# Optimization experiments

Measured on AMD Instinct MI355X. Metric: run time of the kernel, lower is better.

The kernel has to match this reference:

```python
import jax, jax.numpy as jnp
import numpy as np

N_IMG = 512
N_ANGLES = 180


def _bilinear(img, sy, sx):
    """Bilinear sample img at float coords (sy, sx); zero outside the image."""
    n = img.shape[0]
    y0 = jnp.floor(sy)
    x0 = jnp.floor(sx)
    wy = sy - y0
    wx = sx - x0
    y0i = y0.astype(jnp.int32)
    x0i = x0.astype(jnp.int32)

    def gather(yi, xi):
        valid = (yi >= 0) & (yi < n) & (xi >= 0) & (xi < n)
        yc = jnp.clip(yi, 0, n - 1)
        xc = jnp.clip(xi, 0, n - 1)
        return jnp.where(valid, img[yc, xc], jnp.zeros((), img.dtype))

    v00 = gather(y0i, x0i)
    v01 = gather(y0i, x0i + 1)
    v10 = gather(y0i + 1, x0i)
    v11 = gather(y0i + 1, x0i + 1)
    return (v00 * (1 - wy) * (1 - wx) + v01 * (1 - wy) * wx
            + v10 * wy * (1 - wx) + v11 * wy * wx)


def _radon(img, angles):
    """skimage-style radon: rotate image by each angle, sum along axis 0.
    Returns sinogram of shape (n_detectors, n_angles) = (N, len(angles))."""
    n = img.shape[0]
    c = (n - 1) * 0.5  # rotation about image center
    coords = jnp.arange(n, dtype=img.dtype) - c
    yc, xc = jnp.meshgrid(coords, coords, indexing="ij")  # (N, N)

    def one_angle(theta_deg):
        t = jnp.deg2rad(theta_deg.astype(img.dtype))
        co, si = jnp.cos(t), jnp.sin(t)
        # inverse-rotation sampling coordinates (CCW rotation of the image)
        sx = co * xc + si * yc + c
        sy = -si * xc + co * yc + c
        rotated = _bilinear(img, sy, sx)  # (N, N)
        return rotated.sum(axis=0)        # projection along detector rows -> (N,)

    sino = jax.vmap(one_angle)(angles)  # (n_angles, N)
    return sino.T                        # (N, n_angles)


def setup_inputs() -> dict:
    key = jax.random.key(0)
    img = jax.random.uniform(key, (N_IMG, N_IMG), dtype=jnp.float32)  # nonnegative PET activity
    angles = jnp.arange(N_ANGLES, dtype=jnp.int32)  # degrees 0..179 (skimage default)
    return {"img": img, "angles": angles}


def reference(img, angles):
    return _radon(img, angles)
```

## Files before the change

kernel.cpp:

```cpp
#include <hip/hip_runtime.h>
#include <hip/hip_fp16.h>
#include <stdint.h>

#define N 512
#define NA 180
#define TD 64
#define TI 128
#define TW 96
#define TILE_DW (36 * 256)
#define PP 708
#define PR 704
#define POFF 96

#define WS_IMGPB  0
#define WS_IMGTPB (PR * PP)
#define WS_TAB    (2 * PR * PP)
#define WS_FLAGS  (WS_TAB + 4 * NA)
#define WS_OUTT   997888

typedef _Float16 hh2 __attribute__((ext_vector_type(2)));
union H2U { uint32_t u; hh2 h; };

__device__ __forceinline__ hh2 cvt_pkrtz(float a, float b) {
    return __builtin_bit_cast(hh2, __builtin_amdgcn_cvt_pkrtz(a, b));
}

__device__ __forceinline__ void load16_to_lds(const uint32_t* g, uint32_t* l) {
    __builtin_amdgcn_global_load_lds(
        (const __attribute__((address_space(1))) void*)g,
        (__attribute__((address_space(3))) void*)l,
        16 , 0 , 0 );
}

__global__ __launch_bounds__(512) void pad_kernel(const float* __restrict__ img,
                                                  const int* __restrict__ angles,
                                                  uint32_t* __restrict__ imgPB,
                                                  uint32_t* __restrict__ imgTPB,
                                                  float4* __restrict__ tab,
                                                  int* __restrict__ flags,
                                                  float* __restrict__ outT) {
    __shared__ float lds[65 * 66];
    const int tid  = threadIdx.x;
    const int lane = tid & 63;
    const int wq   = tid >> 6;
    const int bx = blockIdx.x, by = blockIdx.y;
    const int b  = by * 11 + bx;

    if (b < 45) {
        float4 z; z.x = z.y = z.z = z.w = 0.0f;
        ((float4*)outT)[b * 512 + tid] = z;
    }
    if (b == 120 && tid < NA) {
        float t = (float)angles[tid] * 0.017453292519943295f;
        float si = sinf(t), co = cosf(t);
        int useT = fabsf(si) > fabsf(co);
        float4 e;
        if (useT) { e.x = co; e.y = -si; e.z = si; e.w = co; }
        else      { e.x = si; e.y = co;  e.z = co; e.w = -si; }
        tab[tid] = e;
        flags[tid] = useT;
    }

    for (int idx = tid; idx < 65 * 65; idx += 512) {
        int r = idx / 65, cc = idx - r * 65;
        int y = by * 64 + r - POFF, x = bx * 64 + cc - POFF;
        bool in = ((unsigned)y < N) && ((unsigned)x < N);
        lds[r * 66 + cc] = in ? img[y * N + x] : 0.0f;
    }
    __syncthreads();
#pragma unroll
    for (int j = 0; j < 8; ++j) {
        int r = wq * 8 + j;
        float v0 = lds[r * 66 + lane], v1 = lds[r * 66 + lane + 1];
        __half2 h = __halves2half2(__float2half(v0), __float2half(v1));
        imgPB[(size_t)(by * 64 + r) * PP + bx * 64 + lane] = *(uint32_t*)&h;
        float t0 = lds[lane * 66 + r], t1 = lds[(lane + 1) * 66 + r];
        __half2 ht = __halves2half2(__float2half(t0), __float2half(t1));
        imgTPB[(size_t)(bx * 64 + r) * PP + by * 64 + lane] = *(uint32_t*)&ht;
    }
}

__global__ __launch_bounds__(512, 8) void radon_kernel(const uint32_t* __restrict__ imgPB,
                                                       const uint32_t* __restrict__ imgTPB,
                                                       const float4* __restrict__ tab,
                                                       const int* __restrict__ flags,
                                                       float* __restrict__ outT) {
    __shared__ uint32_t tile[TILE_DW];

    const int tid  = threadIdx.x;
    const int lane = tid & 63;
    const int wave = tid >> 6;
    const int d0 = blockIdx.x * TD;
    const int a  = blockIdx.y;
    const int i0 = blockIdx.z * TI;

    const float c = 255.5f;
    const float4 tb = tab[a];
    const float au = tb.x, bus = tb.y, av = tb.z, bvs = tb.w;

    const float xc0 = (float)d0 - c, xc1 = (float)(d0 + TD - 1) - c;
    const float buA = fmaf(bus, xc0, c), buB = fmaf(bus, xc1, c);
    const float bvA = fmaf(bvs, xc0, c), bvB = fmaf(bvs, xc1, c);
    const float buMin = fminf(buA, buB), buMax = fmaxf(buA, buB);
    const float bvMin = fminf(bvA, bvB), bvMax = fmaxf(bvA, bvB);

    {
        const float fi0 = (float)i0 - c, fi1 = (float)(i0 + TI - 1) - c;
        const float fiLoU = (au >= 0.0f) ? fi0 : fi1, fiHiU = (au >= 0.0f) ? fi1 : fi0;
        const float fiLoV = (av >= 0.0f) ? fi0 : fi1, fiHiV = (av >= 0.0f) ? fi1 : fi0;
        if (fmaf(au, fiLoU, buMin) > (float)N || fmaf(au, fiHiU, buMax) < -1.0f ||
            fmaf(av, fiLoV, bvMin) > (float)N || fmaf(av, fiHiV, bvMax) < -1.0f)
            return;
    }

    const uint32_t* __restrict__ src = flags[a] ? imgTPB : imgPB;

    const float xcl = (float)(d0 + lane) - c;
    const float buLb = fmaf(bus, xcl, c);
    const float bvLb = fmaf(bvs, xcl, c);

    const int t0g  = wave * 256 + (lane << 2);
    const int q0   = t0g / TW;
    const int c0   = t0g - q0 * TW;
    const int goff0 = q0 * PP + c0;

    float s = 0.0f;
#pragma unroll
    for (int ph = 0; ph < 2; ++ph) {
        const int ip = i0 + ph * 64;
        const float fi0 = (float)ip - c, fi1 = (float)(ip + 63) - c;
        const float fiLoU = (au >= 0.0f) ? fi0 : fi1, fiHiU = (au >= 0.0f) ? fi1 : fi0;
        const float fiLoV = (av >= 0.0f) ? fi0 : fi1, fiHiV = (av >= 0.0f) ? fi1 : fi0;
        const float umin = fmaf(au, fiLoU, buMin), umax = fmaf(au, fiHiU, buMax);
        const float vmin = fmaf(av, fiLoV, bvMin), vmax = fmaf(av, fiHiV, bvMax);
        const bool live = !(umin > (float)N || umax < -1.0f ||
                            vmin > (float)N || vmax < -1.0f);

        const int ub0 = (((int)floorf(umin)) - 1) & ~3;
        const int vb  = ((int)floorf(vmin)) - 1;

        __syncthreads();
        if (live) {
            const uint32_t* gb = src + (vb + POFF) * PP + (ub0 + POFF) + goff0;
            int cc = c0;
#pragma unroll
            for (int st = 0; st < 5; ++st) {
                int chunk = st * 8 + wave;
                if (chunk < 36) load16_to_lds(gb, &tile[chunk * 256]);
                cc += 32;
                int wrap = (cc >= TW);
                cc = wrap ? cc - TW : cc;
                gb += 21 * PP + 32 + (wrap ? (PP - TW) : 0);
            }
        }
        __syncthreads();
        if (live) {
            const float buL = buLb - (float)ub0;
            const float bvL = bvLb - (float)vb;
            const float fiw = (float)(ip + wave * 8) - c;
            float u = fmaf(au, fiw, buL);
            float v = fmaf(av, fiw, bvL);
#pragma unroll
            for (int k = 0; k < 8; ++k) {
                float wx = __builtin_amdgcn_fractf(u);
                float wy = __builtin_amdgcn_fractf(v);
                int iu = (int)u, iv = (int)v;
                int ai = iv * TW + iu;
                H2U P0, P1;
                P0.u = tile[ai];
                P1.u = tile[ai + TW];
                hh2 wy2 = cvt_pkrtz(wy, wy);
                hh2 m   = wy2 * (P1.h - P0.h) + P0.h;
                hh2 wv  = cvt_pkrtz(1.0f - wx, wx);
                s = __builtin_amdgcn_fdot2(wv, m, s, false);
                u += au;
                v += av;
            }
        }
    }

    __syncthreads();
    float* ft = (float*)tile;
    ft[tid] = s;
    __syncthreads();
    if (tid < 64) {
        float r = ft[tid]       + ft[tid + 64]  + ft[tid + 128] + ft[tid + 192]
                + ft[tid + 256] + ft[tid + 320] + ft[tid + 384] + ft[tid + 448];
        atomicAdd(&outT[a * 512 + d0 + tid], r);
    }
}

__global__ __launch_bounds__(256) void txo_kernel(const float* __restrict__ outT,
                                                  float* __restrict__ out) {
    __shared__ float lds[64 * 65];
    const int lane = threadIdx.x & 63;
    const int wq   = threadIdx.x >> 6;
    const int d0 = blockIdx.x * 64;
    const int a0 = blockIdx.y * 64;
#pragma unroll
    for (int j = 0; j < 16; ++j) {
        int r = wq * 16 + j;
        int a = a0 + r;
        lds[r * 65 + lane] = (a < NA) ? outT[a * 512 + d0 + lane] : 0.0f;
    }
    __syncthreads();
#pragma unroll
    for (int j = 0; j < 16; ++j) {
        int r = wq * 16 + j;
        int aa = a0 + lane;
        if (aa < NA) out[(d0 + r) * NA + aa] = lds[lane * 65 + r];
    }
}

extern "C" void kernel_launch(void* const* d_in, const int* in_sizes, int n_in,
                              void* d_out, int out_size, void* d_ws, size_t ws_size,
                              hipStream_t stream) {
    const float* img  = (const float*)d_in[0];
    const int* angles = (const int*)d_in[1];
    float* out = (float*)d_out;
    float* ws  = (float*)d_ws;

    uint32_t* imgPB  = (uint32_t*)(ws + WS_IMGPB);
    uint32_t* imgTPB = (uint32_t*)(ws + WS_IMGTPB);
    float4*   tab    = (float4*)(ws + WS_TAB);
    int*      flags  = (int*)(ws + WS_FLAGS);
    float*    outT   = ws + WS_OUTT;

    dim3 pgrid(11, 11);
    pad_kernel<<<pgrid, 512, 0, stream>>>(img, angles, imgPB, imgTPB, tab, flags, outT);

    dim3 grid(N / TD, NA, N / TI);
    radon_kernel<<<grid, 512, 0, stream>>>(imgPB, imgTPB, tab, flags, outT);

    dim3 tgrid(512 / 64, 3);
    txo_kernel<<<tgrid, 256, 0, stream>>>(outT, out);
}
```

Measured before the change: 97.33 us.

## Drop transpose kernel, atomically accumulate into output directly, double radial tile

The separate transpose kernel is removed and blocks atomically add into the final (detector, angle) layout, with the pad kernel zeroing the output directly. Each block now covers 256 integration rows in four phases instead of 128 in two, halving the number of atomics and blocks. The LDS tile load now fetches only the rows the footprint needs rather than always 36 chunks. Trade-offs: atomics now land at strided addresses, and there are fewer blocks available for parallelism.

```diff
diff --git a/kernel.cpp b/kernel.cpp
--- a/kernel.cpp
+++ b/kernel.cpp
@@ -5,7 +5,7 @@
 #define N 512
 #define NA 180
 #define TD 64
-#define TI 128
+#define TI 256
 #define TW 96
 #define TILE_DW (36 * 256)
 #define PP 708
@@ -16,7 +16,6 @@
 #define WS_IMGTPB (PR * PP)
 #define WS_TAB    (2 * PR * PP)
 #define WS_FLAGS  (WS_TAB + 4 * NA)
-#define WS_OUTT   997888
 
 typedef _Float16 hh2 __attribute__((ext_vector_type(2)));
 union H2U { uint32_t u; hh2 h; };
@@ -38,7 +37,7 @@
                                                   uint32_t* __restrict__ imgTPB,
                                                   float4* __restrict__ tab,
                                                   int* __restrict__ flags,
-                                                  float* __restrict__ outT) {
+                                                  float* __restrict__ out) {
     __shared__ float lds[65 * 66];
     const int tid  = threadIdx.x;
     const int lane = tid & 63;
@@ -48,7 +47,7 @@
 
     if (b < 45) {
         float4 z; z.x = z.y = z.z = z.w = 0.0f;
-        ((float4*)outT)[b * 512 + tid] = z;
+        ((float4*)out)[b * 512 + tid] = z;
     }
     if (b == 120 && tid < NA) {
         float t = (float)angles[tid] * 0.017453292519943295f;
@@ -84,7 +83,7 @@
                                                        const uint32_t* __restrict__ imgTPB,
                                                        const float4* __restrict__ tab,
                                                        const int* __restrict__ flags,
-                                                       float* __restrict__ outT) {
+                                                       float* __restrict__ out) {
     __shared__ uint32_t tile[TILE_DW];
 
     const int tid  = threadIdx.x;
@@ -126,7 +125,7 @@
 
     float s = 0.0f;
 #pragma unroll
-    for (int ph = 0; ph < 2; ++ph) {
+    for (int ph = 0; ph < 4; ++ph) {
         const int ip = i0 + ph * 64;
         const float fi0 = (float)ip - c, fi1 = (float)(ip + 63) - c;
         const float fiLoU = (au >= 0.0f) ? fi0 : fi1, fiHiU = (au >= 0.0f) ? fi1 : fi0;
@@ -138,6 +137,8 @@
 
         const int ub0 = (((int)floorf(umin)) - 1) & ~3;
         const int vb  = ((int)floorf(vmin)) - 1;
+        const int rows = ((int)floorf(vmax)) + 3 - vb;
+        const int nch  = (rows * TW + 255) >> 8;
 
         __syncthreads();
         if (live) {
@@ -146,7 +147,7 @@
 #pragma unroll
             for (int st = 0; st < 5; ++st) {
                 int chunk = st * 8 + wave;
-                if (chunk < 36) load16_to_lds(gb, &tile[chunk * 256]);
+                if (chunk < nch) load16_to_lds(gb, &tile[chunk * 256]);
                 cc += 32;
                 int wrap = (cc >= TW);
                 cc = wrap ? cc - TW : cc;
@@ -186,29 +187,7 @@
     if (tid < 64) {
         float r = ft[tid]       + ft[tid + 64]  + ft[tid + 128] + ft[tid + 192]
                 + ft[tid + 256] + ft[tid + 320] + ft[tid + 384] + ft[tid + 448];
-        atomicAdd(&outT[a * 512 + d0 + tid], r);
-    }
-}
-
-__global__ __launch_bounds__(256) void txo_kernel(const float* __restrict__ outT,
-                                                  float* __restrict__ out) {
-    __shared__ float lds[64 * 65];
-    const int lane = threadIdx.x & 63;
-    const int wq   = threadIdx.x >> 6;
-    const int d0 = blockIdx.x * 64;
-    const int a0 = blockIdx.y * 64;
-#pragma unroll
-    for (int j = 0; j < 16; ++j) {
-        int r = wq * 16 + j;
-        int a = a0 + r;
-        lds[r * 65 + lane] = (a < NA) ? outT[a * 512 + d0 + lane] : 0.0f;
-    }
-    __syncthreads();
-#pragma unroll
-    for (int j = 0; j < 16; ++j) {
-        int r = wq * 16 + j;
-        int aa = a0 + lane;
-        if (aa < NA) out[(d0 + r) * NA + aa] = lds[lane * 65 + r];
+        atomicAdd(&out[(d0 + tid) * NA + a], r);
     }
 }
 
@@ -224,14 +203,10 @@
     uint32_t* imgTPB = (uint32_t*)(ws + WS_IMGTPB);
     float4*   tab    = (float4*)(ws + WS_TAB);
     int*      flags  = (int*)(ws + WS_FLAGS);
-    float*    outT   = ws + WS_OUTT;
 
     dim3 pgrid(11, 11);
-    pad_kernel<<<pgrid, 512, 0, stream>>>(img, angles, imgPB, imgTPB, tab, flags, outT);
+    pad_kernel<<<pgrid, 512, 0, stream>>>(img, angles, imgPB, imgTPB, tab, flags, out);
 
     dim3 grid(N / TD, NA, N / TI);
-    radon_kernel<<<grid, 512, 0, stream>>>(imgPB, imgTPB, tab, flags, outT);
-
-    dim3 tgrid(512 / 64, 3);
-    txo_kernel<<<tgrid, 256, 0, stream>>>(outT, out);
-}
+    radon_kernel<<<grid, 512, 0, stream>>>(imgPB, imgTPB, tab, flags, out);
+}
```

Measured after the change: 92.76 us. -4.7%, faster.
